# Performance work log

Hardware: AMD Instinct MI355X
Metric: run time of the kernel (lower is better)

The kernel has to match this reference:

```python
import jax, jax.numpy as jnp
import numpy as np

N_TOKENS, E, H = 20000, 128, 512
B, T, L = 128, 512, 8


def setup_inputs() -> dict:
    key = jax.random.key(0)
    ks = jax.random.split(key, 9)
    s = 0.02
    return {
        "tokens": jax.random.randint(ks[0], (B, T, L), 0, N_TOKENS),
        "values": jax.random.uniform(ks[1], (B, T, L), dtype=jnp.float32),
        "emb": jax.random.normal(ks[2], (N_TOKENS, E), dtype=jnp.float32) * s,
        "W_ih": jax.random.normal(ks[3], (4 * H, E), dtype=jnp.float32) * s,
        "W_hh": jax.random.normal(ks[4], (4 * H, H), dtype=jnp.float32) * s,
        "b_ih": jnp.zeros((4 * H,), jnp.float32),
        "b_hh": jnp.zeros((4 * H,), jnp.float32),
        "W_out": jax.random.normal(ks[5], (1, H), dtype=jnp.float32) * s,
        "b_out": jnp.zeros((1,), jnp.float32),
    }


def reference(tokens, values, emb, W_ih, W_hh, b_ih, b_hh, W_out, b_out):
    # EmbedTimeseriesW: value-weighted sum of token embeddings per time bin
    e = emb[tokens]                                  # [B,T,L,E]
    x = jnp.einsum('btle,btl->bte', e, values)       # [B,T,E]
    x = jax.nn.relu(x)                               # ReLU (dropout p=0 -> identity)

    xT = jnp.swapaxes(x, 0, 1)                       # [T,B,E]
    b = b_ih + b_hh

    def step(carry, xt):
        h, c = carry
        gates = xt @ W_ih.T + h @ W_hh.T + b         # [B,4H]
        i, f, g, o = jnp.split(gates, 4, axis=-1)    # torch LSTM gate order
        c = jax.nn.sigmoid(f) * c + jax.nn.sigmoid(i) * jnp.tanh(g)
        h = jax.nn.sigmoid(o) * jnp.tanh(c)
        return (h, c), h

    h0 = jnp.zeros((x.shape[0], W_hh.shape[1]), x.dtype)
    (_, _), hs = jax.lax.scan(step, (h0, h0), xT)    # hs: [T,B,H]

    out = jnp.swapaxes(hs, 0, 1) @ W_out.T + b_out   # [B,T,1]
    return out.squeeze(-1)                           # [B,T]
```

## Files before the change

### kernel.cpp

```cpp
#include <hip/hip_runtime.h>
#include <hip/hip_bf16.h>

#define B_   128
#define T_   512
#define L_   8
#define E_   128
#define H_   512

#define BG_   4
#define WPG_  16
#define JW_   32
#define HU64_ (B_ * H_ / 4)
#define GSTR  132

typedef __attribute__((ext_vector_type(8))) short s8v;
typedef __attribute__((ext_vector_type(4))) float f4v;
typedef unsigned long long u64;

__device__ __forceinline__ float bf16u_to_f(unsigned short s) {
  union { unsigned u; float f; } c; c.u = ((unsigned)s) << 16; return c.f;
}
__device__ __forceinline__ u64 llc_load8(const void* p) {
  return __hip_atomic_load((const u64*)p, __ATOMIC_RELAXED, __HIP_MEMORY_SCOPE_AGENT);
}
__device__ __forceinline__ void llc_store8(void* p, u64 v) {
  __hip_atomic_store((u64*)p, v, __ATOMIC_RELAXED, __HIP_MEMORY_SCOPE_AGENT);
}
__device__ __forceinline__ unsigned llc_load4(const unsigned* p) {
  return __hip_atomic_load(p, __ATOMIC_RELAXED, __HIP_MEMORY_SCOPE_AGENT);
}
__device__ __forceinline__ void llc_store4(unsigned* p, unsigned v) {
  __hip_atomic_store(p, v, __ATOMIC_RELAXED, __HIP_MEMORY_SCOPE_AGENT);
}
__device__ __forceinline__ float sigf(float x) {
  return __builtin_amdgcn_rcpf(1.f + __expf(-x));
}
__device__ __forceinline__ float tanh_f(float x) {
  return 1.f - 2.f * __builtin_amdgcn_rcpf(1.f + __expf(2.f * x));
}

__device__ __forceinline__ void wait_flags64(const unsigned* flags, unsigned tgt) {
  const unsigned* p = flags + (threadIdx.x & 63);
  while (!__all((int)(llc_load4(p) >= tgt))) {
    __builtin_amdgcn_s_sleep(1);
  }
}

__global__ void embed_kernel(const int* __restrict__ tokens,
                             const float* __restrict__ values,
                             const float* __restrict__ emb,
                             __hip_bfloat16* __restrict__ x_bf) {
  int idx = blockIdx.x * blockDim.x + threadIdx.x;
  int e  = idx & (E_ - 1);
  int bt = idx >> 7;
  int b  = bt >> 9;
  int t  = bt & (T_ - 1);
  const int*   tok = tokens + (size_t)bt * L_;
  const float* val = values + (size_t)bt * L_;
  float acc = 0.f;
#pragma unroll
  for (int l = 0; l < L_; ++l) acc += emb[(size_t)tok[l] * E_ + e] * val[l];
  acc = fmaxf(acc, 0.f);
  x_bf[((size_t)t * B_ + b) * E_ + e] = __float2bfloat16(acc);
}

__device__ __forceinline__ void out_dot_lds(const u64* __restrict__ h_lds,
                                            int t, int bg,
                                            const float* __restrict__ wout_s,
                                            float bout, float* __restrict__ out) {
  const int um = threadIdx.x >> 3;
  const int uj = threadIdx.x & 7;
  const u64* row = h_lds + (size_t)um * 128;
  const float* wr = wout_s + uj * 64;
  float p = 0.f;
#pragma unroll
  for (int j = 0; j < 8; ++j) {
    int pc = ((uj * 8 + j) ^ (um & 7)) * 2;
    u64 qa = row[pc], qb = row[pc + 1];
    p += bf16u_to_f((unsigned short)(qa      )) * wr[j * 8 + 0];
    p += bf16u_to_f((unsigned short)(qa >> 16)) * wr[j * 8 + 1];
    p += bf16u_to_f((unsigned short)(qa >> 32)) * wr[j * 8 + 2];
    p += bf16u_to_f((unsigned short)(qa >> 48)) * wr[j * 8 + 3];
    p += bf16u_to_f((unsigned short)(qb      )) * wr[j * 8 + 4];
    p += bf16u_to_f((unsigned short)(qb >> 16)) * wr[j * 8 + 5];
    p += bf16u_to_f((unsigned short)(qb >> 32)) * wr[j * 8 + 6];
    p += bf16u_to_f((unsigned short)(qb >> 48)) * wr[j * 8 + 7];
  }
  p += __shfl_down(p, 4, 8);
  p += __shfl_down(p, 2, 8);
  p += __shfl_down(p, 1, 8);
  if (uj == 0) out[(size_t)(bg * 32 + um) * T_ + t] = p + bout;
}

__device__ __forceinline__ void out_dot_glb(const u64* __restrict__ h,
                                            int t, int bg,
                                            const float* __restrict__ wout_s,
                                            float bout, float* __restrict__ out) {
  const int um = threadIdx.x >> 3;
  const int uj = threadIdx.x & 7;
  const int b  = bg * 32 + um;
  const u64* hr = h + (size_t)b * 128 + uj * 16;
  const float* wr = wout_s + uj * 64;
  float p = 0.f;
#pragma unroll
  for (int kk = 0; kk < 16; ++kk) {
    u64 q = llc_load8(hr + kk);
    p += bf16u_to_f((unsigned short)(q      )) * wr[kk * 4 + 0];
    p += bf16u_to_f((unsigned short)(q >> 16)) * wr[kk * 4 + 1];
    p += bf16u_to_f((unsigned short)(q >> 32)) * wr[kk * 4 + 2];
    p += bf16u_to_f((unsigned short)(q >> 48)) * wr[kk * 4 + 3];
  }
  p += __shfl_down(p, 4, 8);
  p += __shfl_down(p, 2, 8);
  p += __shfl_down(p, 1, 8);
  if (uj == 0) out[(size_t)b * T_ + t] = p + bout;
}

__global__ void __launch_bounds__(256, 1)
lstm_kernel(const float* __restrict__ W_ih, const float* __restrict__ W_hh,
            const float* __restrict__ b_ih, const float* __restrict__ b_hh,
            const float* __restrict__ W_out, const float* __restrict__ b_out,
            const __hip_bfloat16* __restrict__ x_bf,
            u64* __restrict__ h_base,
            float* __restrict__ out,
            unsigned* __restrict__ bars) {
  __shared__ __align__(16) u64   h_lds[32 * 128];
  __shared__ __align__(16) float gbuf[32][GSTR];
  __shared__ __align__(16) float bias_s[128];
  __shared__ float wout_s[H_];

  const int tid = threadIdx.x;
  const int wg  = blockIdx.x;
  const int bg  = wg >> 4;
  const int g   = wg & (WPG_ - 1);
  const int j0g = g * JW_;

  const int wv   = tid >> 6;
  const int lane = tid & 63;
  const int m16  = lane & 15;
  const int q    = lane >> 4;
  const int sw   = m16 & 7;

  s8v bfrag[2][20];
#pragma unroll
  for (int nt = 0; nt < 2; ++nt) {
    const int r = wv * H_ + j0g + nt * 16 + m16;
    const float* wih_r = W_ih + (size_t)r * E_;
    const float* whh_r = W_hh + (size_t)r * H_;
#pragma unroll
    for (int ks = 0; ks < 20; ++ks) {
      s8v v;
#pragma unroll
      for (int i = 0; i < 8; ++i) {
        int k = ks * 32 + q * 8 + i;
        float w = (k < E_) ? wih_r[k] : whh_r[k - E_];
        __hip_bfloat16 hb = __float2bfloat16(w);
        v[i] = *(short*)&hb;
      }
      bfrag[nt][ks] = v;
    }
  }
  if (tid < 128) {
    int gt = tid >> 5, jl = tid & 31;
    int r = gt * H_ + j0g + jl;
    bias_s[tid] = b_ih[r] + b_hh[r];
  }
  if (g == 0) for (int i = tid; i < H_; i += 256) wout_s[i] = W_out[i];

  const int um = tid >> 3;
  const int jb = (tid & 7) * 4;
  const int ub = bg * 32 + um;
  const int fc = tid & 7;
  float cst[4] = {0.f, 0.f, 0.f, 0.f};
  const float bout = b_out[0];
  unsigned* flags  = bars + bg * 64;
  unsigned* myflag = flags + (g << 2) + wv;

  int rp = 2, wp = 0;
  f4v acc[2][2];

  {
    const __hip_bfloat16* ax0 = x_bf + (size_t)(bg * 32 + m16) * E_ + q * 8;
    const __hip_bfloat16* ax1 = x_bf + (size_t)(bg * 32 + 16 + m16) * E_ + q * 8;
    f4v z = {0.f, 0.f, 0.f, 0.f};
    acc[0][0] = z; acc[0][1] = z; acc[1][0] = z; acc[1][1] = z;
#pragma unroll
    for (int ks = 0; ks < 4; ++ks) {
      s8v a0 = *(const s8v*)(ax0 + ks * 32);
      s8v a1 = *(const s8v*)(ax1 + ks * 32);
#pragma unroll
      for (int nt = 0; nt < 2; ++nt) {
        acc[0][nt] = __builtin_amdgcn_mfma_f32_16x16x32_bf16(a0, bfrag[nt][ks], acc[0][nt], 0, 0, 0);
        acc[1][nt] = __builtin_amdgcn_mfma_f32_16x16x32_bf16(a1, bfrag[nt][ks], acc[1][nt], 0, 0, 0);
      }
    }
  }
  __syncthreads();

  for (int t = 0; t < T_; ++t) {
    const u64* h_prev = h_base + (size_t)rp * HU64_;
    u64*       h_next = h_base + (size_t)wp * HU64_;

    if (wv == 0) wait_flags64(flags, (unsigned)t);
    __syncthreads();

    {
      const u64* src = h_prev + (size_t)(bg * 32 + um) * 128;
      u64 v[16];
#pragma unroll
      for (int j = 0; j < 8; ++j) {
        int lc = fc + 8 * j;
        v[2 * j]     = llc_load8(src + lc * 2);
        v[2 * j + 1] = llc_load8(src + lc * 2 + 1);
      }
      u64* dst = h_lds + (size_t)um * 128;
#pragma unroll
      for (int j = 0; j < 8; ++j) {
        int pc = ((fc + 8 * j) ^ (um & 7)) * 2;
        dst[pc]     = v[2 * j];
        dst[pc + 1] = v[2 * j + 1];
      }
    }
    __syncthreads();

    {
      const u64* al0 = h_lds + (size_t)m16 * 128;
      const u64* al1 = h_lds + (size_t)(16 + m16) * 128;
#pragma unroll
      for (int ks4 = 0; ks4 < 16; ++ks4) {
        int pc = ((ks4 * 4 + q) ^ sw) * 2;
        s8v a0 = *(const s8v*)(al0 + pc);
        s8v a1 = *(const s8v*)(al1 + pc);
#pragma unroll
        for (int nt = 0; nt < 2; ++nt) {
          acc[0][nt] = __builtin_amdgcn_mfma_f32_16x16x32_bf16(a0, bfrag[nt][4 + ks4], acc[0][nt], 0, 0, 0);
          acc[1][nt] = __builtin_amdgcn_mfma_f32_16x16x32_bf16(a1, bfrag[nt][4 + ks4], acc[1][nt], 0, 0, 0);
        }
      }
    }

#pragma unroll
    for (int mt = 0; mt < 2; ++mt)
#pragma unroll
      for (int nt = 0; nt < 2; ++nt)
#pragma unroll
        for (int r = 0; r < 4; ++r)
          gbuf[mt * 16 + q * 4 + r][wv * 32 + nt * 16 + m16] = acc[mt][nt][r];
    __syncthreads();

    {
      const float* gr = &gbuf[0][0] + (size_t)um * GSTR;
      f4v vi = *(const f4v*)(gr + jb);
      f4v vf = *(const f4v*)(gr + 32 + jb);
      f4v vg = *(const f4v*)(gr + 64 + jb);
      f4v vo = *(const f4v*)(gr + 96 + jb);
      f4v bi = *(const f4v*)(bias_s + jb);
      f4v bf = *(const f4v*)(bias_s + 32 + jb);
      f4v bgc = *(const f4v*)(bias_s + 64 + jb);
      f4v bo = *(const f4v*)(bias_s + 96 + jb);
      u64 packed = 0;
#pragma unroll
      for (int qq = 0; qq < 4; ++qq) {
        float si = sigf(vi[qq] + bi[qq]);
        float sf = sigf(vf[qq] + bf[qq]);
        float tg = tanh_f(vg[qq] + bgc[qq]);
        float so = sigf(vo[qq] + bo[qq]);
        cst[qq] = sf * cst[qq] + si * tg;
        float h = so * tanh_f(cst[qq]);
        __hip_bfloat16 hb = __float2bfloat16(h);
        packed |= (u64)(*(unsigned short*)&hb) << (16 * qq);
      }
      llc_store8(h_next + (size_t)ub * 128 + ((j0g + jb) >> 2), packed);
    }
    asm volatile("s_waitcnt vmcnt(0)" ::: "memory");
    if (lane == 0) llc_store4(myflag, (unsigned)(t + 1));

    if (g == 0 && t > 0)
      out_dot_lds(h_lds, t - 1, bg, wout_s, bout, out);

    if (t + 1 < T_) {
      const __hip_bfloat16* xt = x_bf + (size_t)(t + 1) * B_ * E_;
      const __hip_bfloat16* ax0 = xt + (size_t)(bg * 32 + m16) * E_ + q * 8;
      const __hip_bfloat16* ax1 = xt + (size_t)(bg * 32 + 16 + m16) * E_ + q * 8;
      f4v z = {0.f, 0.f, 0.f, 0.f};
      acc[0][0] = z; acc[0][1] = z; acc[1][0] = z; acc[1][1] = z;
#pragma unroll
      for (int ks = 0; ks < 4; ++ks) {
        s8v a0 = *(const s8v*)(ax0 + ks * 32);
        s8v a1 = *(const s8v*)(ax1 + ks * 32);
#pragma unroll
        for (int nt = 0; nt < 2; ++nt) {
          acc[0][nt] = __builtin_amdgcn_mfma_f32_16x16x32_bf16(a0, bfrag[nt][ks], acc[0][nt], 0, 0, 0);
          acc[1][nt] = __builtin_amdgcn_mfma_f32_16x16x32_bf16(a1, bfrag[nt][ks], acc[1][nt], 0, 0, 0);
        }
      }
    }

    rp = wp; wp = (wp == 2) ? 0 : wp + 1;
  }

  if (g == 0) {
    if (wv == 0) wait_flags64(flags, (unsigned)T_);
    __syncthreads();
    out_dot_glb(h_base + (size_t)rp * HU64_, T_ - 1, bg, wout_s, bout, out);
  }
}

extern "C" void kernel_launch(void* const* d_in, const int* in_sizes, int n_in,
                              void* d_out, int out_size, void* d_ws, size_t ws_size,
                              hipStream_t stream) {
  const int*   tokens = (const int*)d_in[0];
  const float* values = (const float*)d_in[1];
  const float* emb    = (const float*)d_in[2];
  const float* W_ih   = (const float*)d_in[3];
  const float* W_hh   = (const float*)d_in[4];
  const float* b_ih   = (const float*)d_in[5];
  const float* b_hh   = (const float*)d_in[6];
  const float* W_out  = (const float*)d_in[7];
  const float* b_out  = (const float*)d_in[8];
  float* out = (float*)d_out;

  char* ws = (char*)d_ws;
  __hip_bfloat16* x_bf = (__hip_bfloat16*)ws;
  u64* h_base = (u64*)(ws + (size_t)T_ * B_ * E_ * 2);
  unsigned* bars = (unsigned*)(ws + (size_t)T_ * B_ * E_ * 2
                                  + (size_t)3 * HU64_ * sizeof(u64));

  hipMemsetAsync(h_base, 0, (size_t)3 * HU64_ * sizeof(u64), stream);
  hipMemsetAsync(bars, 0, (size_t)BG_ * 64 * sizeof(unsigned), stream);

  embed_kernel<<<(B_ * T_ * E_) / 256, 256, 0, stream>>>(tokens, values, emb, x_bf);

  lstm_kernel<<<dim3(BG_ * WPG_), dim3(256), 0, stream>>>(
      W_ih, W_hh, b_ih, b_hh, W_out, b_out, x_bf, h_base, out, bars);
}
```

Measured before the change: 2.319 ms.

## Replace flag barrier with step-tagged hidden-state words polled directly

Removes the separate per-group flag array and its wait-then-load sequence. Each hidden-state value is now stored in a 32-bit word whose upper half holds the bf16 value and whose lower half holds a step tag, and consumers poll the data itself until the tags match. This cuts out one cross-workgroup round trip per timestep (the vmcnt drain, flag store, and flag poll). In exchange it doubles the hidden-state buffer traffic and adds a per-chunk retry loop with block-wide votes.

```diff
diff --git a/kernel.cpp b/kernel.cpp
--- a/kernel.cpp
+++ b/kernel.cpp
@@ -10,12 +10,14 @@
 #define BG_   4
 #define WPG_  16
 #define JW_   32
-#define HU64_ (B_ * H_ / 4)
+#define HROW_ 512
+#define HBUF_ (B_ * HROW_)
 #define GSTR  132
 
 typedef __attribute__((ext_vector_type(8))) short s8v;
 typedef __attribute__((ext_vector_type(4))) float f4v;
 typedef unsigned long long u64;
+typedef unsigned int u32;
 
 __device__ __forceinline__ float bf16u_to_f(unsigned short s) {
   union { unsigned u; float f; } c; c.u = ((unsigned)s) << 16; return c.f;
@@ -26,24 +28,11 @@
 __device__ __forceinline__ void llc_store8(void* p, u64 v) {
   __hip_atomic_store((u64*)p, v, __ATOMIC_RELAXED, __HIP_MEMORY_SCOPE_AGENT);
 }
-__device__ __forceinline__ unsigned llc_load4(const unsigned* p) {
-  return __hip_atomic_load(p, __ATOMIC_RELAXED, __HIP_MEMORY_SCOPE_AGENT);
-}
-__device__ __forceinline__ void llc_store4(unsigned* p, unsigned v) {
-  __hip_atomic_store(p, v, __ATOMIC_RELAXED, __HIP_MEMORY_SCOPE_AGENT);
-}
 __device__ __forceinline__ float sigf(float x) {
   return __builtin_amdgcn_rcpf(1.f + __expf(-x));
 }
 __device__ __forceinline__ float tanh_f(float x) {
   return 1.f - 2.f * __builtin_amdgcn_rcpf(1.f + __expf(2.f * x));
-}
-
-__device__ __forceinline__ void wait_flags64(const unsigned* flags, unsigned tgt) {
-  const unsigned* p = flags + (threadIdx.x & 63);
-  while (!__all((int)(llc_load4(p) >= tgt))) {
-    __builtin_amdgcn_s_sleep(1);
-  }
 }
 
 __global__ void embed_kernel(const int* __restrict__ tokens,
@@ -92,28 +81,41 @@
   if (uj == 0) out[(size_t)(bg * 32 + um) * T_ + t] = p + bout;
 }
 
-__device__ __forceinline__ void out_dot_glb(const u64* __restrict__ h,
-                                            int t, int bg,
-                                            const float* __restrict__ wout_s,
-                                            float bout, float* __restrict__ out) {
-  const int um = threadIdx.x >> 3;
-  const int uj = threadIdx.x & 7;
-  const int b  = bg * 32 + um;
-  const u64* hr = h + (size_t)b * 128 + uj * 16;
-  const float* wr = wout_s + uj * 64;
-  float p = 0.f;
-#pragma unroll
-  for (int kk = 0; kk < 16; ++kk) {
-    u64 q = llc_load8(hr + kk);
-    p += bf16u_to_f((unsigned short)(q      )) * wr[kk * 4 + 0];
-    p += bf16u_to_f((unsigned short)(q >> 16)) * wr[kk * 4 + 1];
-    p += bf16u_to_f((unsigned short)(q >> 32)) * wr[kk * 4 + 2];
-    p += bf16u_to_f((unsigned short)(q >> 48)) * wr[kk * 4 + 3];
-  }
-  p += __shfl_down(p, 4, 8);
-  p += __shfl_down(p, 2, 8);
-  p += __shfl_down(p, 1, 8);
-  if (uj == 0) out[(size_t)b * T_ + t] = p + bout;
+__device__ __forceinline__ void poll_fill(u64* __restrict__ h_lds,
+                                          const u32* __restrict__ src_row,
+                                          u32 want, int um, int fc) {
+  u64 lo[16], hi[16];
+#pragma unroll
+  for (int jj = 0; jj < 16; ++jj) {
+    const u32* q = src_row + (size_t)(fc + 8 * jj) * 4;
+    lo[jj] = llc_load8(q);
+    hi[jj] = llc_load8(q + 2);
+  }
+  __syncthreads();
+  unsigned miss = 0xffffu;
+  for (;;) {
+#pragma unroll
+    for (int jj = 0; jj < 16; ++jj) if (miss & (1u << jj)) {
+      u32 a0 = (u32)lo[jj], a1 = (u32)(lo[jj] >> 32);
+      u32 a2 = (u32)hi[jj], a3 = (u32)(hi[jj] >> 32);
+      if ((((a0 ^ want) | (a2 ^ want)) & 0xffffu) == 0u) {
+        u64 pk = (u64)((a0 >> 16) | (a1 & 0xffff0000u))
+               | ((u64)((a2 >> 16) | (a3 & 0xffff0000u)) << 32);
+        int qi = fc + 8 * jj;
+        int pc = ((qi >> 1) ^ (um & 7)) * 2 + (qi & 1);
+        h_lds[(size_t)um * 128 + pc] = pk;
+        miss &= ~(1u << jj);
+      }
+    }
+    if (__syncthreads_and((int)(miss == 0u))) break;
+    __builtin_amdgcn_s_sleep(2);
+#pragma unroll
+    for (int jj = 0; jj < 16; ++jj) if (miss & (1u << jj)) {
+      const u32* q = src_row + (size_t)(fc + 8 * jj) * 4;
+      lo[jj] = llc_load8(q);
+      hi[jj] = llc_load8(q + 2);
+    }
+  }
 }
 
 __global__ void __launch_bounds__(256, 1)
@@ -121,9 +123,8 @@
             const float* __restrict__ b_ih, const float* __restrict__ b_hh,
             const float* __restrict__ W_out, const float* __restrict__ b_out,
             const __hip_bfloat16* __restrict__ x_bf,
-            u64* __restrict__ h_base,
-            float* __restrict__ out,
-            unsigned* __restrict__ bars) {
+            u32* __restrict__ h_base,
+            float* __restrict__ out) {
   __shared__ __align__(16) u64   h_lds[32 * 128];
   __shared__ __align__(16) float gbuf[32][GSTR];
   __shared__ __align__(16) float bias_s[128];
@@ -173,8 +174,6 @@
   const int fc = tid & 7;
   float cst[4] = {0.f, 0.f, 0.f, 0.f};
   const float bout = b_out[0];
-  unsigned* flags  = bars + bg * 64;
-  unsigned* myflag = flags + (g << 2) + wv;
 
   int rp = 2, wp = 0;
   f4v acc[2][2];
@@ -195,33 +194,12 @@
       }
     }
   }
-  __syncthreads();
 
   for (int t = 0; t < T_; ++t) {
-    const u64* h_prev = h_base + (size_t)rp * HU64_;
-    u64*       h_next = h_base + (size_t)wp * HU64_;
-
-    if (wv == 0) wait_flags64(flags, (unsigned)t);
-    __syncthreads();
-
-    {
-      const u64* src = h_prev + (size_t)(bg * 32 + um) * 128;
-      u64 v[16];
-#pragma unroll
-      for (int j = 0; j < 8; ++j) {
-        int lc = fc + 8 * j;
-        v[2 * j]     = llc_load8(src + lc * 2);
-        v[2 * j + 1] = llc_load8(src + lc * 2 + 1);
-      }
-      u64* dst = h_lds + (size_t)um * 128;
-#pragma unroll
-      for (int j = 0; j < 8; ++j) {
-        int pc = ((fc + 8 * j) ^ (um & 7)) * 2;
-        dst[pc]     = v[2 * j];
-        dst[pc + 1] = v[2 * j + 1];
-      }
-    }
-    __syncthreads();
+    const u32* h_prev = h_base + (size_t)rp * HBUF_;
+    u32*       h_next = h_base + (size_t)wp * HBUF_;
+
+    poll_fill(h_lds, h_prev + (size_t)ub * HROW_, (u32)t, um, fc);
 
     {
       const u64* al0 = h_lds + (size_t)m16 * 128;
@@ -258,7 +236,8 @@
       f4v bf = *(const f4v*)(bias_s + 32 + jb);
       f4v bgc = *(const f4v*)(bias_s + 64 + jb);
       f4v bo = *(const f4v*)(bias_s + 96 + jb);
-      u64 packed = 0;
+      const u32 tagv = (u32)(t + 1) & 0xffffu;
+      u32 w[4];
 #pragma unroll
       for (int qq = 0; qq < 4; ++qq) {
         float si = sigf(vi[qq] + bi[qq]);
@@ -268,12 +247,12 @@
         cst[qq] = sf * cst[qq] + si * tg;
         float h = so * tanh_f(cst[qq]);
         __hip_bfloat16 hb = __float2bfloat16(h);
-        packed |= (u64)(*(unsigned short*)&hb) << (16 * qq);
-      }
-      llc_store8(h_next + (size_t)ub * 128 + ((j0g + jb) >> 2), packed);
-    }
-    asm volatile("s_waitcnt vmcnt(0)" ::: "memory");
-    if (lane == 0) llc_store4(myflag, (unsigned)(t + 1));
+        w[qq] = ((u32)(*(unsigned short*)&hb) << 16) | ((qq & 1) ? 0u : tagv);
+      }
+      u32* dst = h_next + (size_t)ub * HROW_ + (j0g + jb);
+      llc_store8(dst,     (u64)w[0] | ((u64)w[1] << 32));
+      llc_store8(dst + 2, (u64)w[2] | ((u64)w[3] << 32));
+    }
 
     if (g == 0 && t > 0)
       out_dot_lds(h_lds, t - 1, bg, wout_s, bout, out);
@@ -300,9 +279,9 @@
   }
 
   if (g == 0) {
-    if (wv == 0) wait_flags64(flags, (unsigned)T_);
-    __syncthreads();
-    out_dot_glb(h_base + (size_t)rp * HU64_, T_ - 1, bg, wout_s, bout, out);
+    poll_fill(h_lds, h_base + (size_t)rp * HBUF_ + (size_t)ub * HROW_,
+              (u32)T_, um, fc);
+    out_dot_lds(h_lds, T_ - 1, bg, wout_s, bout, out);
   }
 }
 
@@ -322,15 +301,12 @@
 
   char* ws = (char*)d_ws;
   __hip_bfloat16* x_bf = (__hip_bfloat16*)ws;
-  u64* h_base = (u64*)(ws + (size_t)T_ * B_ * E_ * 2);
-  unsigned* bars = (unsigned*)(ws + (size_t)T_ * B_ * E_ * 2
-                                  + (size_t)3 * HU64_ * sizeof(u64));
-
-  hipMemsetAsync(h_base, 0, (size_t)3 * HU64_ * sizeof(u64), stream);
-  hipMemsetAsync(bars, 0, (size_t)BG_ * 64 * sizeof(unsigned), stream);
+  u32* h_base = (u32*)(ws + (size_t)T_ * B_ * E_ * 2);
+
+  hipMemsetAsync(h_base, 0, (size_t)3 * HBUF_ * sizeof(u32), stream);
 
   embed_kernel<<<(B_ * T_ * E_) / 256, 256, 0, stream>>>(tokens, values, emb, x_bf);
 
   lstm_kernel<<<dim3(BG_ * WPG_), dim3(256), 0, stream>>>(
-      W_ih, W_hh, b_ih, b_hh, W_out, b_out, x_bf, h_base, out, bars);
-}
+      W_ih, W_hh, b_ih, b_hh, W_out, b_out, x_bf, h_base, out);
+}
```

Result: slower. 2.820 ms (+21.6%).

## Split batch into 8 groups with XCC-local fast h exchange via sc0 buffer ops

Applied to the files above, without the earlier changes.

Doubles the workgroup count to 128, each batch group now handling 16 rows instead of 32, and detects at runtime which XCC each workgroup sits on. When all workgroups of a group share an XCC, the hidden state and flags are exchanged through buffer loads and stores with the sc0 bit, meant to stay in the XCC-local L2 instead of going through device-scope coherent memory. A bounded-spin fallback and a duplicated slow path keep correctness otherwise. The cost is double stores every step, extra startup synchronization, and reliance on how the hardware places workgroups.

```diff
diff --git a/kernel.cpp b/kernel.cpp
--- a/kernel.cpp
+++ b/kernel.cpp
@@ -7,15 +7,20 @@
 #define E_   128
 #define H_   512
 
-#define BG_   4
+#define NG_   8
 #define WPG_  16
 #define JW_   32
-#define HU64_ (B_ * H_ / 4)
 #define GSTR  132
+#define HBUFB 131072
+#define BARSA_OFF (3 * HBUFB)
+#define FAST_BYTES (BARSA_OFF + NG_ * 64 * 4)
+#define SPIN_MAX 4096
 
 typedef __attribute__((ext_vector_type(8))) short s8v;
 typedef __attribute__((ext_vector_type(4))) float f4v;
+typedef __attribute__((ext_vector_type(4))) unsigned int u32x4;
 typedef unsigned long long u64;
+typedef unsigned int u32;
 
 __device__ __forceinline__ float bf16u_to_f(unsigned short s) {
   union { unsigned u; float f; } c; c.u = ((unsigned)s) << 16; return c.f;
@@ -23,9 +28,6 @@
 __device__ __forceinline__ u64 llc_load8(const void* p) {
   return __hip_atomic_load((const u64*)p, __ATOMIC_RELAXED, __HIP_MEMORY_SCOPE_AGENT);
 }
-__device__ __forceinline__ void llc_store8(void* p, u64 v) {
-  __hip_atomic_store((u64*)p, v, __ATOMIC_RELAXED, __HIP_MEMORY_SCOPE_AGENT);
-}
 __device__ __forceinline__ unsigned llc_load4(const unsigned* p) {
   return __hip_atomic_load(p, __ATOMIC_RELAXED, __HIP_MEMORY_SCOPE_AGENT);
 }
@@ -39,11 +41,28 @@
   return 1.f - 2.f * __builtin_amdgcn_rcpf(1.f + __expf(2.f * x));
 }
 
-__device__ __forceinline__ void wait_flags64(const unsigned* flags, unsigned tgt) {
-  const unsigned* p = flags + (threadIdx.x & 63);
-  while (!__all((int)(llc_load4(p) >= tgt))) {
+__device__ __forceinline__ void buf_store_sc0(u32x4 srd, unsigned voff, unsigned v) {
+  asm volatile("buffer_store_dword %0, %1, %2, 0 offen sc0"
+               :: "v"(v), "v"(voff), "s"(srd) : "memory");
+}
+__device__ __forceinline__ unsigned buf_load_sc0(u32x4 srd, unsigned voff) {
+  unsigned v;
+  asm volatile("buffer_load_dword %0, %1, %2, 0 offen sc0\n\ts_waitcnt vmcnt(0)"
+               : "=v"(v) : "v"(voff), "s"(srd) : "memory");
+  return v;
+}
+
+__device__ __forceinline__ bool wait_flags_fast(u32x4 srd, unsigned polloff, unsigned tgt) {
+  for (int it = 0; it < SPIN_MAX; ++it) {
+    unsigned v = buf_load_sc0(srd, polloff);
+    if (__all((int)(v >= tgt))) return true;
     __builtin_amdgcn_s_sleep(1);
   }
+  return false;
+}
+__device__ __forceinline__ void wait_flags_slow(const u32* flags, unsigned tgt) {
+  const u32* p = flags + (threadIdx.x & 63);
+  while (!__all((int)(llc_load4(p) >= tgt))) __builtin_amdgcn_s_sleep(1);
 }
 
 __global__ void embed_kernel(const int* __restrict__ tokens,
@@ -64,18 +83,53 @@
   x_bf[((size_t)t * B_ + b) * E_ + e] = __float2bfloat16(acc);
 }
 
-__device__ __forceinline__ void out_dot_lds(const u64* __restrict__ h_lds,
-                                            int t, int bg,
-                                            const float* __restrict__ wout_s,
-                                            float bout, float* __restrict__ out) {
-  const int um = threadIdx.x >> 3;
-  const int uj = threadIdx.x & 7;
-  const u64* row = h_lds + (size_t)um * 128;
-  const float* wr = wout_s + uj * 64;
+__device__ __forceinline__ void fill_slab(u32x4* __restrict__ h_lds4, int mode,
+                                          u32x4 srd, unsigned voffA,
+                                          const u64* __restrict__ slow_src,
+                                          int tid) {
+  u32x4 c0, c1, c2, c3;
+  if (mode == 0) {
+    asm volatile(
+        "buffer_load_dwordx4 %0, %4, %5, 0 offen sc0\n\t"
+        "buffer_load_dwordx4 %1, %4, %5, 0 offen offset:16 sc0\n\t"
+        "buffer_load_dwordx4 %2, %4, %5, 0 offen offset:32 sc0\n\t"
+        "buffer_load_dwordx4 %3, %4, %5, 0 offen offset:48 sc0\n\t"
+        "s_waitcnt vmcnt(0)"
+        : "=&v"(c0), "=&v"(c1), "=&v"(c2), "=&v"(c3)
+        : "v"(voffA), "s"(srd) : "memory");
+  } else {
+    u64 a, b;
+    a = llc_load8(slow_src + 0); b = llc_load8(slow_src + 1);
+    c0 = (u32x4){(u32)a, (u32)(a >> 32), (u32)b, (u32)(b >> 32)};
+    a = llc_load8(slow_src + 2); b = llc_load8(slow_src + 3);
+    c1 = (u32x4){(u32)a, (u32)(a >> 32), (u32)b, (u32)(b >> 32)};
+    a = llc_load8(slow_src + 4); b = llc_load8(slow_src + 5);
+    c2 = (u32x4){(u32)a, (u32)(a >> 32), (u32)b, (u32)(b >> 32)};
+    a = llc_load8(slow_src + 6); b = llc_load8(slow_src + 7);
+    c3 = (u32x4){(u32)a, (u32)(a >> 32), (u32)b, (u32)(b >> 32)};
+  }
+  const int row = tid >> 4;
+  const int sw2 = row & 7;
+  const int cb  = (tid & 15) * 4;
+  u32x4* dst = h_lds4 + (size_t)row * 64;
+  dst[(cb + 0) ^ sw2] = c0;
+  dst[(cb + 1) ^ sw2] = c1;
+  dst[(cb + 2) ^ sw2] = c2;
+  dst[(cb + 3) ^ sw2] = c3;
+}
+
+__device__ __forceinline__ void out_dot_lds16(const u32x4* __restrict__ h_lds4,
+                                              int t, int gid,
+                                              const float* __restrict__ wout_s,
+                                              float bout, float* __restrict__ out) {
+  const int um = threadIdx.x >> 4;
+  const int uj = threadIdx.x & 15;
+  const u64* row = (const u64*)(h_lds4 + (size_t)um * 64);
+  const float* wr = wout_s + uj * 32;
   float p = 0.f;
 #pragma unroll
-  for (int j = 0; j < 8; ++j) {
-    int pc = ((uj * 8 + j) ^ (um & 7)) * 2;
+  for (int j = 0; j < 4; ++j) {
+    int pc = ((uj * 4 + j) ^ (um & 7)) * 2;
     u64 qa = row[pc], qb = row[pc + 1];
     p += bf16u_to_f((unsigned short)(qa      )) * wr[j * 8 + 0];
     p += bf16u_to_f((unsigned short)(qa >> 16)) * wr[j * 8 + 1];
@@ -86,34 +140,11 @@
     p += bf16u_to_f((unsigned short)(qb >> 32)) * wr[j * 8 + 6];
     p += bf16u_to_f((unsigned short)(qb >> 48)) * wr[j * 8 + 7];
   }
-  p += __shfl_down(p, 4, 8);
-  p += __shfl_down(p, 2, 8);
-  p += __shfl_down(p, 1, 8);
-  if (uj == 0) out[(size_t)(bg * 32 + um) * T_ + t] = p + bout;
-}
-
-__device__ __forceinline__ void out_dot_glb(const u64* __restrict__ h,
-                                            int t, int bg,
-                                            const float* __restrict__ wout_s,
-                                            float bout, float* __restrict__ out) {
-  const int um = threadIdx.x >> 3;
-  const int uj = threadIdx.x & 7;
-  const int b  = bg * 32 + um;
-  const u64* hr = h + (size_t)b * 128 + uj * 16;
-  const float* wr = wout_s + uj * 64;
-  float p = 0.f;
-#pragma unroll
-  for (int kk = 0; kk < 16; ++kk) {
-    u64 q = llc_load8(hr + kk);
-    p += bf16u_to_f((unsigned short)(q      )) * wr[kk * 4 + 0];
-    p += bf16u_to_f((unsigned short)(q >> 16)) * wr[kk * 4 + 1];
-    p += bf16u_to_f((unsigned short)(q >> 32)) * wr[kk * 4 + 2];
-    p += bf16u_to_f((unsigned short)(q >> 48)) * wr[kk * 4 + 3];
-  }
-  p += __shfl_down(p, 4, 8);
-  p += __shfl_down(p, 2, 8);
-  p += __shfl_down(p, 1, 8);
-  if (uj == 0) out[(size_t)b * T_ + t] = p + bout;
+  p += __shfl_down(p, 8, 16);
+  p += __shfl_down(p, 4, 16);
+  p += __shfl_down(p, 2, 16);
+  p += __shfl_down(p, 1, 16);
+  if (uj == 0) out[(size_t)(gid * 16 + um) * T_ + t] = p + bout;
 }
 
 __global__ void __launch_bounds__(256, 1)
@@ -121,18 +152,21 @@
             const float* __restrict__ b_ih, const float* __restrict__ b_hh,
             const float* __restrict__ W_out, const float* __restrict__ b_out,
             const __hip_bfloat16* __restrict__ x_bf,
-            u64* __restrict__ h_base,
+            u64* __restrict__ h_slow,
             float* __restrict__ out,
-            unsigned* __restrict__ bars) {
-  __shared__ __align__(16) u64   h_lds[32 * 128];
-  __shared__ __align__(16) float gbuf[32][GSTR];
+            u32* __restrict__ barsB,
+            u32* __restrict__ xcc_tab,
+            char* __restrict__ fastbase) {
+  __shared__ __align__(16) u32x4 h_lds4[16 * 64];
+  __shared__ __align__(16) float gbuf[16][GSTR];
   __shared__ __align__(16) float bias_s[128];
   __shared__ float wout_s[H_];
+  __shared__ int   cnt_same_s, bad_grp_s, mode_s;
 
   const int tid = threadIdx.x;
   const int wg  = blockIdx.x;
-  const int bg  = wg >> 4;
-  const int g   = wg & (WPG_ - 1);
+  const int gid = wg & (NG_ - 1);
+  const int g   = wg >> 3;
   const int j0g = g * JW_;
 
   const int wv   = tid >> 6;
@@ -141,6 +175,25 @@
   const int q    = lane >> 4;
   const int sw   = m16 & 7;
 
+  u32x4 srd;
+  {
+    unsigned long long ba = (unsigned long long)fastbase;
+    srd = (u32x4){(u32)ba, (u32)(ba >> 32) & 0xffffu, 0xffffffffu, 0x00020000u};
+  }
+
+  const unsigned xcc = (unsigned)__builtin_amdgcn_s_getreg(20 | (3 << 11));
+  if (tid == 0) { cnt_same_s = 0; bad_grp_s = 0; llc_store4(xcc_tab + wg, xcc + 1u); }
+  __syncthreads();
+  if (tid < 128) {
+    const u32* slot = xcc_tab + tid;
+    unsigned v = llc_load4(slot);
+    while (v == 0u) { __builtin_amdgcn_s_sleep(8); v = llc_load4(slot); }
+    if (v == xcc + 1u) atomicAdd(&cnt_same_s, 1);
+    else if ((tid & 7) == gid) bad_grp_s = 1;
+  }
+  __syncthreads();
+  if (tid == 0) mode_s = ((bad_grp_s == 0) && (cnt_same_s <= 64)) ? 0 : 1;
+
   s8v bfrag[2][20];
 #pragma unroll
   for (int nt = 0; nt < 2; ++nt) {
@@ -167,132 +220,112 @@
   }
   if (g == 0) for (int i = tid; i < H_; i += 256) wout_s[i] = W_out[i];
 
-  const int um = tid >> 3;
-  const int jb = (tid & 7) * 4;
-  const int ub = bg * 32 + um;
-  const int fc = tid & 7;
-  float cst[4] = {0.f, 0.f, 0.f, 0.f};
+  const int um = tid >> 4;
+  const int jb = (tid & 15) * 2;
+  const int ub = gid * 16 + um;
+  float cst[2] = {0.f, 0.f};
   const float bout = b_out[0];
-  unsigned* flags  = bars + bg * 64;
-  unsigned* myflag = flags + (g << 2) + wv;
+  u32* h_slow32 = (u32*)h_slow;
+  u32* flagsB   = barsB + gid * 64;
+  u32* myflagB  = flagsB + (g << 2) + wv;
+  const unsigned hoffA_base  = (unsigned)(ub * 1024 + (g * 16 + (tid & 15)) * 4);
+  const unsigned hslow_base  = (unsigned)(ub * 256 + g * 16 + (tid & 15));
+  const unsigned flagAoff    = (unsigned)(BARSA_OFF + (gid * 64 + (g << 2) + wv) * 4);
+  const unsigned polloff     = (unsigned)(BARSA_OFF + (gid * 64 + (tid & 63)) * 4);
+  const unsigned filloffA    = (unsigned)((gid * 16 + (tid >> 4)) * 1024 + (tid & 15) * 64);
+  const unsigned slab_u64off = (unsigned)(gid * 16 * 128 + tid * 8);
 
   int rp = 2, wp = 0;
-  f4v acc[2][2];
+  f4v acc[2];
 
   {
-    const __hip_bfloat16* ax0 = x_bf + (size_t)(bg * 32 + m16) * E_ + q * 8;
-    const __hip_bfloat16* ax1 = x_bf + (size_t)(bg * 32 + 16 + m16) * E_ + q * 8;
+    const __hip_bfloat16* ax0 = x_bf + (size_t)(gid * 16 + m16) * E_ + q * 8;
     f4v z = {0.f, 0.f, 0.f, 0.f};
-    acc[0][0] = z; acc[0][1] = z; acc[1][0] = z; acc[1][1] = z;
+    acc[0] = z; acc[1] = z;
 #pragma unroll
     for (int ks = 0; ks < 4; ++ks) {
       s8v a0 = *(const s8v*)(ax0 + ks * 32);
-      s8v a1 = *(const s8v*)(ax1 + ks * 32);
-#pragma unroll
-      for (int nt = 0; nt < 2; ++nt) {
-        acc[0][nt] = __builtin_amdgcn_mfma_f32_16x16x32_bf16(a0, bfrag[nt][ks], acc[0][nt], 0, 0, 0);
-        acc[1][nt] = __builtin_amdgcn_mfma_f32_16x16x32_bf16(a1, bfrag[nt][ks], acc[1][nt], 0, 0, 0);
-      }
+#pragma unroll
+      for (int nt = 0; nt < 2; ++nt)
+        acc[nt] = __builtin_amdgcn_mfma_f32_16x16x32_bf16(a0, bfrag[nt][ks], acc[nt], 0, 0, 0);
     }
   }
   __syncthreads();
 
   for (int t = 0; t < T_; ++t) {
-    const u64* h_prev = h_base + (size_t)rp * HU64_;
-    u64*       h_next = h_base + (size_t)wp * HU64_;
-
-    if (wv == 0) wait_flags64(flags, (unsigned)t);
+    if (wv == 0) {
+      int m0 = mode_s;
+      bool got = false;
+      if (m0 == 0) {
+        got = wait_flags_fast(srd, polloff, (unsigned)t);
+        if (!got && lane == 0) mode_s = 1;
+      }
+      if (!got) wait_flags_slow(flagsB, (unsigned)t);
+    }
+    __syncthreads();
+    const int mode = mode_s;
+
+    fill_slab(h_lds4, mode, srd, (unsigned)(rp * HBUFB) + filloffA,
+              h_slow + (size_t)rp * 16384 + slab_u64off, tid);
     __syncthreads();
 
     {
-      const u64* src = h_prev + (size_t)(bg * 32 + um) * 128;
-      u64 v[16];
-#pragma unroll
-      for (int j = 0; j < 8; ++j) {
-        int lc = fc + 8 * j;
-        v[2 * j]     = llc_load8(src + lc * 2);
-        v[2 * j + 1] = llc_load8(src + lc * 2 + 1);
-      }
-      u64* dst = h_lds + (size_t)um * 128;
-#pragma unroll
-      for (int j = 0; j < 8; ++j) {
-        int pc = ((fc + 8 * j) ^ (um & 7)) * 2;
-        dst[pc]     = v[2 * j];
-        dst[pc + 1] = v[2 * j + 1];
-      }
-    }
+      const s8v* arow = (const s8v*)(h_lds4 + (size_t)m16 * 64);
+#pragma unroll
+      for (int ks4 = 0; ks4 < 16; ++ks4) {
+        s8v a0 = arow[(ks4 * 4 + q) ^ sw];
+#pragma unroll
+        for (int nt = 0; nt < 2; ++nt)
+          acc[nt] = __builtin_amdgcn_mfma_f32_16x16x32_bf16(a0, bfrag[nt][4 + ks4], acc[nt], 0, 0, 0);
+      }
+    }
+
+#pragma unroll
+    for (int nt = 0; nt < 2; ++nt)
+#pragma unroll
+      for (int r = 0; r < 4; ++r)
+        gbuf[q * 4 + r][wv * 32 + nt * 16 + m16] = acc[nt][r];
     __syncthreads();
 
     {
-      const u64* al0 = h_lds + (size_t)m16 * 128;
-      const u64* al1 = h_lds + (size_t)(16 + m16) * 128;
-#pragma unroll
-      for (int ks4 = 0; ks4 < 16; ++ks4) {
-        int pc = ((ks4 * 4 + q) ^ sw) * 2;
-        s8v a0 = *(const s8v*)(al0 + pc);
-        s8v a1 = *(const s8v*)(al1 + pc);
-#pragma unroll
-        for (int nt = 0; nt < 2; ++nt) {
-          acc[0][nt] = __builtin_amdgcn_mfma_f32_16x16x32_bf16(a0, bfrag[nt][4 + ks4], acc[0][nt], 0, 0, 0);
-          acc[1][nt] = __builtin_amdgcn_mfma_f32_16x16x32_bf16(a1, bfrag[nt][4 + ks4], acc[1][nt], 0, 0, 0);
-        }
-      }
-    }
-
-#pragma unroll
-    for (int mt = 0; mt < 2; ++mt)
-#pragma unroll
-      for (int nt = 0; nt < 2; ++nt)
-#pragma unroll
-        for (int r = 0; r < 4; ++r)
-          gbuf[mt * 16 + q * 4 + r][wv * 32 + nt * 16 + m16] = acc[mt][nt][r];
-    __syncthreads();
-
-    {
-      const float* gr = &gbuf[0][0] + (size_t)um * GSTR;
-      f4v vi = *(const f4v*)(gr + jb);
-      f4v vf = *(const f4v*)(gr + 32 + jb);
-      f4v vg = *(const f4v*)(gr + 64 + jb);
-      f4v vo = *(const f4v*)(gr + 96 + jb);
-      f4v bi = *(const f4v*)(bias_s + jb);
-      f4v bf = *(const f4v*)(bias_s + 32 + jb);
-      f4v bgc = *(const f4v*)(bias_s + 64 + jb);
-      f4v bo = *(const f4v*)(bias_s + 96 + jb);
-      u64 packed = 0;
-#pragma unroll
-      for (int qq = 0; qq < 4; ++qq) {
-        float si = sigf(vi[qq] + bi[qq]);
-        float sf = sigf(vf[qq] + bf[qq]);
-        float tg = tanh_f(vg[qq] + bgc[qq]);
-        float so = sigf(vo[qq] + bo[qq]);
-        cst[qq] = sf * cst[qq] + si * tg;
-        float h = so * tanh_f(cst[qq]);
-        __hip_bfloat16 hb = __float2bfloat16(h);
-        packed |= (u64)(*(unsigned short*)&hb) << (16 * qq);
-      }
-      llc_store8(h_next + (size_t)ub * 128 + ((j0g + jb) >> 2), packed);
-    }
-    asm volatile("s_waitcnt vmcnt(0)" ::: "memory");
-    if (lane == 0) llc_store4(myflag, (unsigned)(t + 1));
+      const float* gr = &gbuf[um][0];
+      float si0 = sigf(gr[jb]      + bias_s[jb]);
+      float si1 = sigf(gr[jb + 1]  + bias_s[jb + 1]);
+      float sf0 = sigf(gr[32 + jb] + bias_s[32 + jb]);
+      float sf1 = sigf(gr[33 + jb] + bias_s[33 + jb]);
+      float tg0 = tanh_f(gr[64 + jb] + bias_s[64 + jb]);
+      float tg1 = tanh_f(gr[65 + jb] + bias_s[65 + jb]);
+      float so0 = sigf(gr[96 + jb] + bias_s[96 + jb]);
+      float so1 = sigf(gr[97 + jb] + bias_s[97 + jb]);
+      cst[0] = sf0 * cst[0] + si0 * tg0;
+      cst[1] = sf1 * cst[1] + si1 * tg1;
+      float h0 = so0 * tanh_f(cst[0]);
+      float h1 = so1 * tanh_f(cst[1]);
+      __hip_bfloat16 hb0 = __float2bfloat16(h0);
+      __hip_bfloat16 hb1 = __float2bfloat16(h1);
+      u32 w = (u32)(*(unsigned short*)&hb0) | ((u32)(*(unsigned short*)&hb1) << 16);
+      buf_store_sc0(srd, (unsigned)(wp * HBUFB) + hoffA_base, w);
+      llc_store4(h_slow32 + (size_t)wp * 32768 + hslow_base, w);
+      asm volatile("s_waitcnt vmcnt(1)" ::: "memory");
+      if (lane == 0) buf_store_sc0(srd, flagAoff, (unsigned)(t + 1));
+      asm volatile("s_waitcnt vmcnt(0)" ::: "memory");
+      if (lane == 0) llc_store4(myflagB, (unsigned)(t + 1));
+    }
 
     if (g == 0 && t > 0)
-      out_dot_lds(h_lds, t - 1, bg, wout_s, bout, out);
+      out_dot_lds16(h_lds4, t - 1, gid, wout_s, bout, out);
 
     if (t + 1 < T_) {
       const __hip_bfloat16* xt = x_bf + (size_t)(t + 1) * B_ * E_;
-      const __hip_bfloat16* ax0 = xt + (size_t)(bg * 32 + m16) * E_ + q * 8;
-      const __hip_bfloat16* ax1 = xt + (size_t)(bg * 32 + 16 + m16) * E_ + q * 8;
+      const __hip_bfloat16* ax0 = xt + (size_t)(gid * 16 + m16) * E_ + q * 8;
       f4v z = {0.f, 0.f, 0.f, 0.f};
-      acc[0][0] = z; acc[0][1] = z; acc[1][0] = z; acc[1][1] = z;
+      acc[0] = z; acc[1] = z;
 #pragma unroll
       for (int ks = 0; ks < 4; ++ks) {
         s8v a0 = *(const s8v*)(ax0 + ks * 32);
-        s8v a1 = *(const s8v*)(ax1 + ks * 32);
-#pragma unroll
-        for (int nt = 0; nt < 2; ++nt) {
-          acc[0][nt] = __builtin_amdgcn_mfma_f32_16x16x32_bf16(a0, bfrag[nt][ks], acc[0][nt], 0, 0, 0);
-          acc[1][nt] = __builtin_amdgcn_mfma_f32_16x16x32_bf16(a1, bfrag[nt][ks], acc[1][nt], 0, 0, 0);
-        }
+#pragma unroll
+        for (int nt = 0; nt < 2; ++nt)
+          acc[nt] = __builtin_amdgcn_mfma_f32_16x16x32_bf16(a0, bfrag[nt][ks], acc[nt], 0, 0, 0);
       }
     }
 
@@ -300,9 +333,20 @@
   }
 
   if (g == 0) {
-    if (wv == 0) wait_flags64(flags, (unsigned)T_);
-    __syncthreads();
-    out_dot_glb(h_base + (size_t)rp * HU64_, T_ - 1, bg, wout_s, bout, out);
+    if (wv == 0) {
+      int m0 = mode_s;
+      bool got = false;
+      if (m0 == 0) {
+        got = wait_flags_fast(srd, polloff, (unsigned)T_);
+        if (!got && lane == 0) mode_s = 1;
+      }
+      if (!got) wait_flags_slow(flagsB, (unsigned)T_);
+    }
+    __syncthreads();
+    fill_slab(h_lds4, mode_s, srd, (unsigned)(rp * HBUFB) + filloffA,
+              h_slow + (size_t)rp * 16384 + slab_u64off, tid);
+    __syncthreads();
+    out_dot_lds16(h_lds4, T_ - 1, gid, wout_s, bout, out);
   }
 }
 
@@ -322,15 +366,17 @@
 
   char* ws = (char*)d_ws;
   __hip_bfloat16* x_bf = (__hip_bfloat16*)ws;
-  u64* h_base = (u64*)(ws + (size_t)T_ * B_ * E_ * 2);
-  unsigned* bars = (unsigned*)(ws + (size_t)T_ * B_ * E_ * 2
-                                  + (size_t)3 * HU64_ * sizeof(u64));
-
-  hipMemsetAsync(h_base, 0, (size_t)3 * HU64_ * sizeof(u64), stream);
-  hipMemsetAsync(bars, 0, (size_t)BG_ * 64 * sizeof(unsigned), stream);
+  char* p = ws + (size_t)T_ * B_ * E_ * 2;
+  u64*  h_slow  = (u64*)p;
+  u32*  barsB   = (u32*)(p + 3 * HBUFB);
+  u32*  xcc_tab = (u32*)(p + 3 * HBUFB + 2048);
+  char* fastbase = p + 3 * HBUFB + 2048 + 512;
+
+  hipMemsetAsync(p, 0, (size_t)(3 * HBUFB + 2048 + 512) + FAST_BYTES, stream);
 
   embed_kernel<<<(B_ * T_ * E_) / 256, 256, 0, stream>>>(tokens, values, emb, x_bf);
 
-  lstm_kernel<<<dim3(BG_ * WPG_), dim3(256), 0, stream>>>(
-      W_ih, W_hh, b_ih, b_hh, W_out, b_out, x_bf, h_base, out, bars);
-}
+  lstm_kernel<<<dim3(NG_ * WPG_), dim3(256), 0, stream>>>(
+      W_ih, W_hh, b_ih, b_hh, W_out, b_out, x_bf, h_slow, out, barsB, xcc_tab,
+      fastbase);
+}
```

Result: faster. 2.073 ms (-10.6%).
